# Optimization experiments

Measured on AMD Instinct MI355X. Metric: run time of the kernel, lower is better.

Reference implementation:

```python
import jax, jax.numpy as jnp
import numpy as np

B, T, D, H, E, K = 4, 1024, 1024, 2048, 8, 2  # batch, tokens, model_dim, ffn hidden, experts, top-k


def setup_inputs() -> dict:
    key = jax.random.key(0)
    k0, k1, k2, k3 = jax.random.split(key, 4)
    return {
        "x": jax.random.normal(k0, (B, T, D), dtype=jnp.float32),
        "wg": jax.random.normal(k1, (D, E), dtype=jnp.float32) * 0.02,   # gate projection
        "w1": jax.random.normal(k2, (E, D, H), dtype=jnp.float32) * 0.02,  # expert fc1
        "b1": jnp.zeros((E, H), dtype=jnp.float32),
        "w2": jax.random.normal(k3, (E, H, D), dtype=jnp.float32) * 0.02,  # expert fc2
        "b2": jnp.zeros((E, D), dtype=jnp.float32),
    }


def _moe(x, wg, w1, b1, w2, b2):
    N = B * T
    xt = x.reshape(N, D)
    # --- gating: softmax scores, top-2 selection, normalize selected gates ---
    logits = xt @ wg                         # [N, E]
    scores = jax.nn.softmax(logits, axis=-1)
    vals, idx = jax.lax.top_k(scores, K)     # [N, K]
    vals = vals / jnp.sum(vals, axis=-1, keepdims=True)
    # combine weights: [N, E], nonzero only at the top-k experts per token
    combine = jnp.zeros((N, E), dtype=xt.dtype).at[
        jnp.arange(N)[:, None], idx
    ].add(vals)
    # --- expert FFN (activation_fn is identity per source) ---
    h = jnp.einsum('nd,edh->neh', xt, w1) + b1   # [N, E, H]
    o = jnp.einsum('neh,ehd->ned', h, w2) + b2   # [N, E, D]
    # --- combine / scatter back ---
    y = jnp.einsum('ne,ned->nd', combine, o)     # [N, D]
    return y.reshape(B, T, D)


def reference(x, wg, w1, b1, w2, b2):
    y = _moe(x, wg, w1, b1, w2, b2)              # [B, T, D]
    s = jnp.sum(y, axis=2)                       # [B, T]
    return jax.nn.log_softmax(s, axis=1)
```

## Files before the change

kernel.cpp:

```cpp
#include <hip/hip_runtime.h>
#include <stdint.h>

#define B_ 4
#define T_ 1024
#define D_ 1024
#define H_ 2048
#define E_ 8

__device__ __forceinline__ void stage16(const float* g, float* l) {
    __builtin_amdgcn_global_load_lds(
        (const __attribute__((address_space(1))) uint32_t*)g,
        (__attribute__((address_space(3))) uint32_t*)l, 16, 0, 0);
}

__global__ __launch_bounds__(256) void w2sum_kernel(const float* __restrict__ w2,
                                                    float* __restrict__ w2sum) {
    __shared__ float buf[3][4 * D_];
    const int wid = threadIdx.x >> 6, lane = threadIdx.x & 63;
    const float* src = w2 + ((size_t)blockIdx.x * 32 + wid) * D_ + lane * 4;

#define A_STAGE(k)                                                        \
    {                                                                     \
        const float* s_ = src + (size_t)(k) * 4 * D_;                     \
        float* d_ = &buf[(k) % 3][wid * D_];                              \
        stage16(s_,       d_);       stage16(s_ + 256, d_ + 256);         \
        stage16(s_ + 512, d_ + 512); stage16(s_ + 768, d_ + 768);         \
    }

    A_STAGE(0); A_STAGE(1);
    float accs[8];
#pragma unroll
    for (int k = 0; k < 8; ++k) {
        if (k < 7) asm volatile("s_waitcnt vmcnt(4)" ::: "memory");
        else       asm volatile("s_waitcnt vmcnt(0)" ::: "memory");
        if (k < 6) A_STAGE(k + 2);
        const float* row = &buf[k % 3][wid * D_];
        float acc = 0.f;
#pragma unroll
        for (int j = 0; j < 4; ++j) {
            float4 a = *(const float4*)&row[j * 256 + lane * 4];
            acc += a.x + a.y + a.z + a.w;
        }
#pragma unroll
        for (int off = 32; off >= 1; off >>= 1) acc += __shfl_xor(acc, off, 64);
        accs[k] = acc;
    }
#undef A_STAGE
    if (lane == 0) {
        const int r0 = blockIdx.x * 32 + wid;
#pragma unroll
        for (int k = 0; k < 8; ++k) w2sum[r0 + k * 4] = accs[k];
    }
}

__global__ __launch_bounds__(256) void v_build_kernel(const float* __restrict__ w1,
                                                      const float* __restrict__ w2sum,
                                                      const float* __restrict__ b1,
                                                      const float* __restrict__ b2,
                                                      float* __restrict__ vT,
                                                      float* __restrict__ c) {
    __shared__ float buf[2][4 * H_];
    const int bid = blockIdx.x;
    const int e   = bid >> 6;
    const int d0  = (bid & 63) * 16;
    const int wid = threadIdx.x >> 6, lane = threadIdx.x & 63;
    const float* src = w1 + ((size_t)e * D_ + d0 + wid) * H_ + lane * 4;

    const float4* wsp = (const float4*)(w2sum + (size_t)e * H_) + lane;
    float4 s0 = wsp[0],   s1 = wsp[64],  s2 = wsp[128], s3 = wsp[192],
           s4 = wsp[256], s5 = wsp[320], s6 = wsp[384], s7 = wsp[448];
    asm volatile("" ::: "memory");

#define B_STAGE(k)                                                         \
    {                                                                      \
        const float* s_ = src + (size_t)(k) * 4 * H_;                      \
        float* d_ = &buf[(k) & 1][wid * H_];                               \
        stage16(s_,        d_);        stage16(s_ + 256,  d_ + 256);       \
        stage16(s_ + 512,  d_ + 512);  stage16(s_ + 768,  d_ + 768);       \
        stage16(s_ + 1024, d_ + 1024); stage16(s_ + 1280, d_ + 1280);      \
        stage16(s_ + 1536, d_ + 1536); stage16(s_ + 1792, d_ + 1792);      \
    }

    B_STAGE(0); B_STAGE(1);
    float accs[4];
#pragma unroll
    for (int k = 0; k < 4; ++k) {
        if (k < 3) asm volatile("s_waitcnt vmcnt(8)" ::: "memory");
        else       asm volatile("s_waitcnt vmcnt(0)" ::: "memory");
        const float* row = &buf[k & 1][wid * H_];
        float acc;
        {
            float4 a0 = *(const float4*)&row[0 * 256 + lane * 4];
            float4 a1 = *(const float4*)&row[1 * 256 + lane * 4];
            float4 a2 = *(const float4*)&row[2 * 256 + lane * 4];
            float4 a3 = *(const float4*)&row[3 * 256 + lane * 4];
            float4 a4 = *(const float4*)&row[4 * 256 + lane * 4];
            float4 a5 = *(const float4*)&row[5 * 256 + lane * 4];
            float4 a6 = *(const float4*)&row[6 * 256 + lane * 4];
            float4 a7 = *(const float4*)&row[7 * 256 + lane * 4];
            acc = a0.x*s0.x + a0.y*s0.y + a0.z*s0.z + a0.w*s0.w
                + a1.x*s1.x + a1.y*s1.y + a1.z*s1.z + a1.w*s1.w
                + a2.x*s2.x + a2.y*s2.y + a2.z*s2.z + a2.w*s2.w
                + a3.x*s3.x + a3.y*s3.y + a3.z*s3.z + a3.w*s3.w
                + a4.x*s4.x + a4.y*s4.y + a4.z*s4.z + a4.w*s4.w
                + a5.x*s5.x + a5.y*s5.y + a5.z*s5.z + a5.w*s5.w
                + a6.x*s6.x + a6.y*s6.y + a6.z*s6.z + a6.w*s6.w
                + a7.x*s7.x + a7.y*s7.y + a7.z*s7.z + a7.w*s7.w;
        }
#pragma unroll
        for (int off = 32; off >= 1; off >>= 1) acc += __shfl_xor(acc, off, 64);
        accs[k] = acc;
        if (k < 2) B_STAGE(k + 2);
    }
#undef B_STAGE
    if (lane == 0) {
#pragma unroll
        for (int k = 0; k < 4; ++k)
            vT[(size_t)(d0 + k * 4 + wid) * E_ + e] = accs[k];
    }

    if ((bid & 63) == 0 && wid == 0) {
        const float4* bp = (const float4*)(b1 + (size_t)e * H_) + lane;
        float4 q0 = bp[0],   q1 = bp[64],  q2 = bp[128], q3 = bp[192],
               q4 = bp[256], q5 = bp[320], q6 = bp[384], q7 = bp[448];
        float s = q0.x*s0.x + q0.y*s0.y + q0.z*s0.z + q0.w*s0.w
                + q1.x*s1.x + q1.y*s1.y + q1.z*s1.z + q1.w*s1.w
                + q2.x*s2.x + q2.y*s2.y + q2.z*s2.z + q2.w*s2.w
                + q3.x*s3.x + q3.y*s3.y + q3.z*s3.z + q3.w*s3.w
                + q4.x*s4.x + q4.y*s4.y + q4.z*s4.z + q4.w*s4.w
                + q5.x*s5.x + q5.y*s5.y + q5.z*s5.z + q5.w*s5.w
                + q6.x*s6.x + q6.y*s6.y + q6.z*s6.z + q6.w*s6.w
                + q7.x*s7.x + q7.y*s7.y + q7.z*s7.z + q7.w*s7.w;
        const float4* cp = (const float4*)(b2 + (size_t)e * D_) + lane;
#pragma unroll
        for (int j = 0; j < 4; ++j) {
            float4 bb = cp[j * 64];
            s += bb.x + bb.y + bb.z + bb.w;
        }
#pragma unroll
        for (int off = 32; off >= 1; off >>= 1) s += __shfl_xor(s, off, 64);
        if (lane == 0) c[e] = s;
    }
}

__global__ __launch_bounds__(256) void token_kernel(
    const float* __restrict__ x,  const float* __restrict__ wg,
    const float* __restrict__ vT, const float* __restrict__ cbuf,
    float* __restrict__ sbuf)
{
    __shared__ float wgl[D_ * E_];
    __shared__ float vtl[D_ * E_];
    const int wid = threadIdx.x >> 6, lane = threadIdx.x & 63;

#pragma unroll
    for (int r = 0; r < 8; ++r) {
        int base = r * 1024 + wid * 256;
        stage16(wg + base + lane * 4, wgl + base);
        stage16(vT + base + lane * 4, vtl + base);
    }
    asm volatile("s_waitcnt vmcnt(0)" ::: "memory");
    __syncthreads();

    const int half = lane & 1;
    const int rrow = lane >> 1;

    const int nA = blockIdx.x * 8 + wid * 2;
    const float* xga = x + (size_t)nA * D_ + rrow;
    const float* xgb = xga + D_;

    float agA[4] = {0,0,0,0}, avA[4] = {0,0,0,0};
    float agB[4] = {0,0,0,0}, avB[4] = {0,0,0,0};

#pragma unroll
    for (int k = 0; k < 32; ++k) {
        float xa = xga[32 * k];
        float xb = xgb[32 * k];
        const int o = (32 * k + rrow) * 8 + half * 4;
        float4 w4 = *(const float4*)&wgl[o];
        float4 v4 = *(const float4*)&vtl[o];
        agA[0] += xa * w4.x; agA[1] += xa * w4.y; agA[2] += xa * w4.z; agA[3] += xa * w4.w;
        avA[0] += xa * v4.x; avA[1] += xa * v4.y; avA[2] += xa * v4.z; avA[3] += xa * v4.w;
        agB[0] += xb * w4.x; agB[1] += xb * w4.y; agB[2] += xb * w4.z; agB[3] += xb * w4.w;
        avB[0] += xb * v4.x; avB[1] += xb * v4.y; avB[2] += xb * v4.z; avB[3] += xb * v4.w;
    }

#pragma unroll
    for (int off = 2; off <= 32; off <<= 1) {
#pragma unroll
        for (int q = 0; q < 4; ++q) {
            agA[q] += __shfl_xor(agA[q], off, 64);
            avA[q] += __shfl_xor(avA[q], off, 64);
            agB[q] += __shfl_xor(agB[q], off, 64);
            avB[q] += __shfl_xor(avB[q], off, 64);
        }
    }
    float gA4 = __shfl(agA[0], 1, 64), gA5 = __shfl(agA[1], 1, 64),
          gA6 = __shfl(agA[2], 1, 64), gA7 = __shfl(agA[3], 1, 64);
    float hA4 = __shfl(avA[0], 1, 64), hA5 = __shfl(avA[1], 1, 64),
          hA6 = __shfl(avA[2], 1, 64), hA7 = __shfl(avA[3], 1, 64);
    float gB4 = __shfl(agB[0], 1, 64), gB5 = __shfl(agB[1], 1, 64),
          gB6 = __shfl(agB[2], 1, 64), gB7 = __shfl(agB[3], 1, 64);
    float hB4 = __shfl(avB[0], 1, 64), hB5 = __shfl(avB[1], 1, 64),
          hB6 = __shfl(avB[2], 1, 64), hB7 = __shfl(avB[3], 1, 64);

    if (lane == 0) {
#pragma unroll
        for (int tok = 0; tok < 2; ++tok) {
            float lg[E_], dv[E_];
            if (tok == 0) {
                lg[0]=agA[0]; lg[1]=agA[1]; lg[2]=agA[2]; lg[3]=agA[3];
                lg[4]=gA4;    lg[5]=gA5;    lg[6]=gA6;    lg[7]=gA7;
                dv[0]=avA[0]; dv[1]=avA[1]; dv[2]=avA[2]; dv[3]=avA[3];
                dv[4]=hA4;    dv[5]=hA5;    dv[6]=hA6;    dv[7]=hA7;
            } else {
                lg[0]=agB[0]; lg[1]=agB[1]; lg[2]=agB[2]; lg[3]=agB[3];
                lg[4]=gB4;    lg[5]=gB5;    lg[6]=gB6;    lg[7]=gB7;
                dv[0]=avB[0]; dv[1]=avB[1]; dv[2]=avB[2]; dv[3]=avB[3];
                dv[4]=hB4;    dv[5]=hB5;    dv[6]=hB6;    dv[7]=hB7;
            }
            float m0 = lg[0]; int i0 = 0;
#pragma unroll
            for (int q = 1; q < E_; ++q) if (lg[q] > m0) { m0 = lg[q]; i0 = q; }
            float m1 = -3.0e38f; int i1 = 0;
#pragma unroll
            for (int q = 0; q < E_; ++q) if (q != i0 && lg[q] > m1) { m1 = lg[q]; i1 = q; }
            float dv0 = 0.f, dv1 = 0.f, c0v = 0.f, c1v = 0.f;
#pragma unroll
            for (int q = 0; q < E_; ++q) {
                if (q == i0) { dv0 += dv[q]; c0v += cbuf[q]; }
                if (q == i1) { dv1 += dv[q]; c1v += cbuf[q]; }
            }
            float g1w = 1.f / (1.f + expf(m0 - m1));
            sbuf[nA + tok] = (1.f - g1w) * (dv0 + c0v) + g1w * (dv1 + c1v);
        }
    }
}

__global__ __launch_bounds__(256) void lsm_kernel(const float* __restrict__ s,
                                                  float* __restrict__ out) {
    int brow = threadIdx.x >> 6;
    int lane = threadIdx.x & 63;
    const float* row = s + (size_t)brow * T_;
    float vals[16];
    float mx = -3.0e38f;
#pragma unroll
    for (int k = 0; k < 16; ++k) {
        vals[k] = row[lane + 64 * k];
        mx = fmaxf(mx, vals[k]);
    }
#pragma unroll
    for (int off = 32; off >= 1; off >>= 1) mx = fmaxf(mx, __shfl_xor(mx, off, 64));
    float sm = 0.f;
#pragma unroll
    for (int k = 0; k < 16; ++k) sm += expf(vals[k] - mx);
#pragma unroll
    for (int off = 32; off >= 1; off >>= 1) sm += __shfl_xor(sm, off, 64);
    float lse = mx + logf(sm);
#pragma unroll
    for (int k = 0; k < 16; ++k) out[(size_t)brow * T_ + lane + 64 * k] = vals[k] - lse;
}

extern "C" void kernel_launch(void* const* d_in, const int* in_sizes, int n_in,
                              void* d_out, int out_size, void* d_ws, size_t ws_size,
                              hipStream_t stream) {
    const float* x  = (const float*)d_in[0];
    const float* wg = (const float*)d_in[1];
    const float* w1 = (const float*)d_in[2];
    const float* b1 = (const float*)d_in[3];
    const float* w2 = (const float*)d_in[4];
    const float* b2 = (const float*)d_in[5];
    float* out = (float*)d_out;

    float* ws     = (float*)d_ws;
    float* w2sum  = ws;
    float* vT     = ws + 16384;
    float* cbuf   = ws + 24576;
    float* sbuf   = ws + 24592;

    w2sum_kernel<<<dim3(512), dim3(256), 0, stream>>>(w2, w2sum);
    v_build_kernel<<<dim3(512), dim3(256), 0, stream>>>(w1, w2sum, b1, b2, vT, cbuf);
    token_kernel<<<dim3(512), dim3(256), 0, stream>>>(x, wg, vT, cbuf, sbuf);
    lsm_kernel<<<dim3(1), dim3(256), 0, stream>>>(sbuf, out);
}
```

Measured before the change: 38.75 us.

## Fuse w2sum and v_build kernels with per-expert atomic counter sync

Merges the w2 row-sum kernel and the v-build kernel into one launch. Blocks of each expert signal completion through a global atomic counter and spin until all 64 blocks for that expert are done, then read w2sum with cache-bypassing loads into shared memory. This removes one kernel launch boundary and lets experts proceed independently, at the cost of a memset launch, spin-wait overhead and a reliance on all 512 blocks being co-resident to avoid deadlock.

```diff
diff --git a/kernel.cpp b/kernel.cpp
--- a/kernel.cpp
+++ b/kernel.cpp
@@ -7,69 +7,97 @@
 #define H_ 2048
 #define E_ 8
 
+#define AL(p)    __hip_atomic_load((p), __ATOMIC_RELAXED, __HIP_MEMORY_SCOPE_AGENT)
+#define AS(p, v) __hip_atomic_store((p), (v), __ATOMIC_RELAXED, __HIP_MEMORY_SCOPE_AGENT)
+
 __device__ __forceinline__ void stage16(const float* g, float* l) {
     __builtin_amdgcn_global_load_lds(
         (const __attribute__((address_space(1))) uint32_t*)g,
         (__attribute__((address_space(3))) uint32_t*)l, 16, 0, 0);
 }
 
-__global__ __launch_bounds__(256) void w2sum_kernel(const float* __restrict__ w2,
-                                                    float* __restrict__ w2sum) {
-    __shared__ float buf[3][4 * D_];
+__device__ __forceinline__ void load2x16_sc(const float* p0, const float* p1,
+                                            float4& r0, float4& r1) {
+    asm volatile(
+        "global_load_dwordx4 %0, %2, off sc0 sc1\n\t"
+        "global_load_dwordx4 %1, %3, off sc0 sc1\n\t"
+        "s_waitcnt vmcnt(0)"
+        : "=&v"(r0), "=&v"(r1)
+        : "v"(p0), "v"(p1)
+        : "memory");
+}
+
+__global__ __launch_bounds__(256) void ab_kernel(
+    const float* __restrict__ w1, const float* __restrict__ b1,
+    const float* __restrict__ w2, const float* __restrict__ b2,
+    float* __restrict__ w2sum, float* __restrict__ vT,
+    float* __restrict__ cbuf, unsigned* __restrict__ ecnt)
+{
+    __shared__ float buf[2][4 * H_];
+    __shared__ float wssum[H_];
+    const int bid = blockIdx.x;
+    const int e   = bid >> 6;
     const int wid = threadIdx.x >> 6, lane = threadIdx.x & 63;
-    const float* src = w2 + ((size_t)blockIdx.x * 32 + wid) * D_ + lane * 4;
-
+
+    {
+        float* abuf = &buf[0][0];
+        const float* src = w2 + ((size_t)bid * 32 + wid) * D_ + lane * 4;
 #define A_STAGE(k)                                                        \
     {                                                                     \
         const float* s_ = src + (size_t)(k) * 4 * D_;                     \
-        float* d_ = &buf[(k) % 3][wid * D_];                              \
+        float* d_ = abuf + ((k) % 3) * 4096 + wid * D_;                   \
         stage16(s_,       d_);       stage16(s_ + 256, d_ + 256);         \
         stage16(s_ + 512, d_ + 512); stage16(s_ + 768, d_ + 768);         \
     }
-
-    A_STAGE(0); A_STAGE(1);
-    float accs[8];
-#pragma unroll
-    for (int k = 0; k < 8; ++k) {
-        if (k < 7) asm volatile("s_waitcnt vmcnt(4)" ::: "memory");
-        else       asm volatile("s_waitcnt vmcnt(0)" ::: "memory");
-        if (k < 6) A_STAGE(k + 2);
-        const float* row = &buf[k % 3][wid * D_];
-        float acc = 0.f;
-#pragma unroll
-        for (int j = 0; j < 4; ++j) {
-            float4 a = *(const float4*)&row[j * 256 + lane * 4];
-            acc += a.x + a.y + a.z + a.w;
-        }
-#pragma unroll
-        for (int off = 32; off >= 1; off >>= 1) acc += __shfl_xor(acc, off, 64);
-        accs[k] = acc;
-    }
+        A_STAGE(0); A_STAGE(1);
+        float accs[8];
+#pragma unroll
+        for (int k = 0; k < 8; ++k) {
+            if (k < 7) asm volatile("s_waitcnt vmcnt(4)" ::: "memory");
+            else       asm volatile("s_waitcnt vmcnt(0)" ::: "memory");
+            if (k < 6) A_STAGE(k + 2);
+            const float* row = abuf + (k % 3) * 4096 + wid * D_;
+            float acc = 0.f;
+#pragma unroll
+            for (int j = 0; j < 4; ++j) {
+                float4 a = *(const float4*)&row[j * 256 + lane * 4];
+                acc += a.x + a.y + a.z + a.w;
+            }
+#pragma unroll
+            for (int off = 32; off >= 1; off >>= 1) acc += __shfl_xor(acc, off, 64);
+            accs[k] = acc;
+        }
 #undef A_STAGE
-    if (lane == 0) {
-        const int r0 = blockIdx.x * 32 + wid;
-#pragma unroll
-        for (int k = 0; k < 8; ++k) w2sum[r0 + k * 4] = accs[k];
-    }
-}
-
-__global__ __launch_bounds__(256) void v_build_kernel(const float* __restrict__ w1,
-                                                      const float* __restrict__ w2sum,
-                                                      const float* __restrict__ b1,
-                                                      const float* __restrict__ b2,
-                                                      float* __restrict__ vT,
-                                                      float* __restrict__ c) {
-    __shared__ float buf[2][4 * H_];
-    const int bid = blockIdx.x;
-    const int e   = bid >> 6;
-    const int d0  = (bid & 63) * 16;
-    const int wid = threadIdx.x >> 6, lane = threadIdx.x & 63;
+        if (lane == 0) {
+            const int r0 = bid * 32 + wid;
+#pragma unroll
+            for (int k = 0; k < 8; ++k) AS(&w2sum[r0 + k * 4], accs[k]);
+        }
+    }
+    asm volatile("s_waitcnt vmcnt(0)" ::: "memory");
+    __syncthreads();
+    if (threadIdx.x == 0)
+        __hip_atomic_fetch_add(&ecnt[e], 1u, __ATOMIC_RELAXED, __HIP_MEMORY_SCOPE_AGENT);
+
+    if (threadIdx.x == 0)
+        while (AL(&ecnt[e]) < 64u) __builtin_amdgcn_s_sleep(2);
+    __syncthreads();
+
+    {
+        const float* wsg = w2sum + (size_t)e * H_ + threadIdx.x * 4;
+        float4 r0, r1;
+        load2x16_sc(wsg, wsg + 1024, r0, r1);
+        *(float4*)&wssum[threadIdx.x * 4]        = r0;
+        *(float4*)&wssum[threadIdx.x * 4 + 1024] = r1;
+    }
+    __syncthreads();
+
+    const int d0 = (bid & 63) * 16;
     const float* src = w1 + ((size_t)e * D_ + d0 + wid) * H_ + lane * 4;
 
-    const float4* wsp = (const float4*)(w2sum + (size_t)e * H_) + lane;
+    const float4* wsp = (const float4*)wssum + lane;
     float4 s0 = wsp[0],   s1 = wsp[64],  s2 = wsp[128], s3 = wsp[192],
            s4 = wsp[256], s5 = wsp[320], s6 = wsp[384], s7 = wsp[448];
-    asm volatile("" ::: "memory");
 
 #define B_STAGE(k)                                                         \
     {                                                                      \
@@ -139,7 +167,7 @@
         }
 #pragma unroll
         for (int off = 32; off >= 1; off >>= 1) s += __shfl_xor(s, off, 64);
-        if (lane == 0) c[e] = s;
+        if (lane == 0) cbuf[e] = s;
     }
 }
 
@@ -276,9 +304,12 @@
     float* vT     = ws + 16384;
     float* cbuf   = ws + 24576;
     float* sbuf   = ws + 24592;
-
-    w2sum_kernel<<<dim3(512), dim3(256), 0, stream>>>(w2, w2sum);
-    v_build_kernel<<<dim3(512), dim3(256), 0, stream>>>(w1, w2sum, b1, b2, vT, cbuf);
+    unsigned* ecnt = (unsigned*)(ws + 28688);
+
+    hipMemsetAsync(ecnt, 0, E_ * sizeof(unsigned), stream);
+
+    ab_kernel<<<dim3(512), dim3(256), 0, stream>>>(
+        w1, b1, w2, b2, w2sum, vT, cbuf, ecnt);
     token_kernel<<<dim3(512), dim3(256), 0, stream>>>(x, wg, vT, cbuf, sbuf);
     lsm_kernel<<<dim3(1), dim3(256), 0, stream>>>(sbuf, out);
 }
```

New measurement: 55.65 us. 43.6% more time.
